# Kernel tuning notes

Measured on AMD Instinct MI355X. Metric: run time of the kernel, lower is better.

The kernel has to match this reference:

```python
import jax, jax.numpy as jnp
import numpy as np

N = 50000      # cells (nodes)
E = 800000     # kNN edges
IN = 50        # PCA dims
HID = 64       # hidden_dim
HEADS = 4
C = HID // HEADS  # per-head channels = 16
L = 3          # num_layers
NC = 12        # num_classes
INV_SQRT_C = 1.0 / np.sqrt(C)
LN_EPS = 1e-5


def setup_inputs() -> dict:
    key = jax.random.key(0)
    ks = iter(jax.random.split(key, 32))
    def w(shape, fan_in):
        return jax.random.normal(next(ks), shape, jnp.float32) / np.sqrt(fan_in)
    inp = {
        'x': jax.random.normal(next(ks), (N, IN), jnp.float32),
        'edge_index': jax.random.randint(next(ks), (2, E), 0, N, jnp.int32),
        'edge_attr': jax.random.uniform(next(ks), (E,), jnp.float32),
        # input projection
        'Win': w((IN, HID), IN), 'b_in': jnp.zeros((HID,), jnp.float32),
        # per-layer TransformerConv params (stacked over L)
        'Wq': w((L, HID, HID), HID), 'bq': jnp.zeros((L, HID), jnp.float32),
        'Wk': w((L, HID, HID), HID), 'bk': jnp.zeros((L, HID), jnp.float32),
        'Wv': w((L, HID, HID), HID), 'bv': jnp.zeros((L, HID), jnp.float32),
        'Wedge': w((L, 1, HID), 1),                      # lin_edge, bias=False
        'Wskip': w((L, HID, HID), HID), 'bskip': jnp.zeros((L, HID), jnp.float32),
        'Wbeta': w((L, 3 * HID, 1), 3 * HID),            # lin_beta, bias=False
        'ln_g': jnp.ones((L, HID), jnp.float32), 'ln_b': jnp.zeros((L, HID), jnp.float32),
        # classifier MLP
        'Wc1': w((HID, HID), HID), 'bc1': jnp.zeros((HID,), jnp.float32),
        'Wc2': w((HID, NC), HID), 'bc2': jnp.zeros((NC,), jnp.float32),
    }
    return inp


def _layer_norm(z, g, b):
    mu = z.mean(-1, keepdims=True)
    var = ((z - mu) ** 2).mean(-1, keepdims=True)
    return (z - mu) / jnp.sqrt(var + LN_EPS) * g + b


def reference(x, edge_index, edge_attr, Win, b_in, Wq, bq, Wk, bk, Wv, bv,
              Wedge, Wskip, bskip, Wbeta, ln_g, ln_b, Wc1, bc1, Wc2, bc2):
    n = x.shape[0]
    src, dst = edge_index[0], edge_index[1]   # messages flow src -> dst
    ea = edge_attr[:, None]                    # (E,1)
    h = x @ Win + b_in                         # (N,HID)
    for i in range(L):
        h_res = h
        q = (h @ Wq[i] + bq[i]).reshape(n, HEADS, C)
        k = (h @ Wk[i] + bk[i]).reshape(n, HEADS, C)
        v = (h @ Wv[i] + bv[i]).reshape(n, HEADS, C)
        e = (ea @ Wedge[i]).reshape(-1, HEADS, C)        # (E,H,C)
        kj = k[src] + e                                   # edge-gathered keys + edge feat
        alpha = jnp.einsum('ehc,ehc->eh', q[dst], kj) * INV_SQRT_C  # (E,H)
        # segment softmax over destination nodes
        amax = jax.ops.segment_max(alpha, dst, num_segments=n)
        amax = jnp.where(jnp.isfinite(amax), amax, 0.0)
        ex = jnp.exp(alpha - amax[dst])
        denom = jax.ops.segment_sum(ex, dst, num_segments=n)
        p = ex / (denom[dst] + 1e-16)
        msg = (v[src] + e) * p[..., None]                 # (E,H,C)
        out = jax.ops.segment_sum(msg, dst, num_segments=n).reshape(n, HID)
        # beta-gated skip
        x_r = h @ Wskip[i] + bskip[i]
        beta = jax.nn.sigmoid(jnp.concatenate([out, x_r, out - x_r], -1) @ Wbeta[i])  # (N,1)
        out = beta * x_r + (1.0 - beta) * out
        h = _layer_norm(out + h_res, ln_g[i], ln_b[i])
    h1 = jax.nn.relu(h @ Wc1 + bc1)
    return h1 @ Wc2 + bc2
```

## Files before the change

### kernel.cpp

```cpp
#include <hip/hip_runtime.h>
#include <hip/hip_fp16.h>
#include <math.h>

#define IN_F 50
#define HID 64
#define NC 12
#define LN_EPS 1e-5f

#define BSH 8
#define BSZ 256
#define NBK_MAX 256
#define CHUNK 8192
#define PCAP 8192

#define SCQ 0.36067376022224085f

typedef _Float16 half8 __attribute__((ext_vector_type(8)));
typedef _Float16 half4_t __attribute__((ext_vector_type(4)));
typedef _Float16 half2_t __attribute__((ext_vector_type(2)));
typedef float float4v __attribute__((ext_vector_type(4)));

static __device__ __forceinline__ half2_t h2cast(unsigned int u) {
  return __builtin_bit_cast(half2_t, u);
}

#if __has_builtin(__builtin_amdgcn_fdot2)
#define FDOT2(a, b, c) __builtin_amdgcn_fdot2((a), (b), (c), false)
#else
static __device__ __forceinline__ float FDOT2(half2_t a, half2_t b, float c) {
  return (float)a[0] * (float)b[0] + (float)a[1] * (float)b[1] + c;
}
#endif


__global__ __launch_bounds__(256) void bucket_kernel(
    const int* __restrict__ src, const int* __restrict__ dst,
    const float* __restrict__ ea, int* __restrict__ cursor,
    unsigned long long* __restrict__ rec_stage,
    unsigned short* __restrict__ dloc_stage, int e)
{
  __shared__ int bcnt[256];
  __shared__ int gbase[256];
  __shared__ int bfill[256];
  int tid = threadIdx.x;
  bcnt[tid] = 0; bfill[tid] = 0;
  __syncthreads();
  int cb = blockIdx.x * CHUNK;
  int ce = min(cb + CHUNK, e);
  for (int i = cb + tid; i < ce; i += 256)
    atomicAdd(&bcnt[dst[i] >> BSH], 1);
  __syncthreads();
  if (bcnt[tid] > 0) gbase[tid] = atomicAdd(&cursor[tid], bcnt[tid]);
  __syncthreads();
  for (int i = cb + tid; i < ce; i += 256) {
    int d = dst[i];
    int b = d >> BSH;
    int slot = atomicAdd(&bfill[b], 1);
    size_t pos = (size_t)b * PCAP + gbase[b] + slot;
    rec_stage[pos] =
        ((unsigned long long)__float_as_uint(ea[i]) << 32) | (unsigned int)src[i];
    dloc_stage[pos] = (unsigned short)(d & (BSZ - 1));
  }
}

__global__ __launch_bounds__(256) void scanb_kernel(
    const int* __restrict__ cursor, int* __restrict__ bbase,
    int* __restrict__ rowptr_n, int nbk)
{
  int t = threadIdx.x;
  int v = (t < nbk) ? cursor[t] : 0;
  int incl = v;
#pragma unroll
  for (int off = 1; off < 64; off <<= 1) {
    int tv = __shfl_up(incl, off);
    if ((t & 63) >= off) incl += tv;
  }
  __shared__ int ws[4];
  if ((t & 63) == 63) ws[t >> 6] = incl;
  __syncthreads();
  int wb = 0;
  int w = t >> 6;
#pragma unroll
  for (int j = 0; j < 4; j++) if (j < w) wb += ws[j];
  int excl = incl - v + wb;
  if (t < nbk) bbase[t] = excl;
  if (t == 255) *rowptr_n = excl;
}

__global__ __launch_bounds__(256) void place_kernel(
    const int* __restrict__ cursor, const int* __restrict__ bbase,
    const unsigned long long* __restrict__ rec_stage,
    const unsigned short* __restrict__ dloc_stage,
    unsigned long long* __restrict__ edges, int* __restrict__ rowptr, int n)
{
  extern __shared__ char smem[];
  unsigned long long* sbuf = (unsigned long long*)smem;
  int* hist = (int*)(smem + (size_t)PCAP * 8);
  int* lcnt = hist + 256;
  __shared__ int ws[4];
  int b = blockIdx.x;
  int t = threadIdx.x;
  int lo = b * BSZ;
  int hi = min(lo + BSZ, n);
  int cnt  = cursor[b];
  int base = bbase[b];
  size_t bofs = (size_t)b * PCAP;
  hist[t] = 0;
  __syncthreads();
  for (int i = t; i < cnt; i += 256)
    atomicAdd(&hist[dloc_stage[bofs + i]], 1);
  __syncthreads();
  int v = hist[t];
  int incl = v;
#pragma unroll
  for (int off = 1; off < 64; off <<= 1) {
    int tv = __shfl_up(incl, off);
    if ((t & 63) >= off) incl += tv;
  }
  if ((t & 63) == 63) ws[t >> 6] = incl;
  __syncthreads();
  int wb = 0;
  int w = t >> 6;
#pragma unroll
  for (int j = 0; j < 4; j++) if (j < w) wb += ws[j];
  int excl = incl - v + wb;
  if (lo + t < hi) rowptr[lo + t] = base + excl;
  lcnt[t] = excl;
  __syncthreads();
  for (int i = t; i < cnt; i += 256) {
    unsigned long long rec = rec_stage[bofs + i];
    int dl = dloc_stage[bofs + i];
    int slot = atomicAdd(&lcnt[dl], 1);
    sbuf[slot] = rec;
  }
  __syncthreads();
  for (int i = t; i < cnt; i += 256)
    edges[(size_t)base + i] = sbuf[i];
}


__global__ __launch_bounds__(256) void wprep_kernel(
    const float* __restrict__ Wq, const float* __restrict__ Wk,
    const float* __restrict__ Wv, const float* __restrict__ Ws,
    const float* __restrict__ Wc1, const float* __restrict__ Win,
    const float* __restrict__ bq, const float* __restrict__ bk,
    const float* __restrict__ bv, const float* __restrict__ bs,
    const float* __restrict__ bc1, const float* __restrict__ bin,
    _Float16* __restrict__ Wt, float* __restrict__ biasP)
{
  int idx = blockIdx.x * 256 + threadIdx.x;
  if (idx >= 896 * 64) return;
  int col = idx >> 6, k = idx & 63;
  float w, b;
  if (col < 768) {
    int l = col >> 8, rem = col & 255;
    int mat = rem >> 6, c = rem & 63;
    const float* W  = (mat == 0) ? Wq : (mat == 1) ? Wk : (mat == 2) ? Wv : Ws;
    const float* bb = (mat == 0) ? bq : (mat == 1) ? bk : (mat == 2) ? bv : bs;
    w = W[((size_t)l * 64 + k) * 64 + c];
    b = bb[l * 64 + c];
  } else if (col < 832) {
    int c = col - 768;
    w = Wc1[k * 64 + c];
    b = bc1[c];
  } else {
    int c = col - 832;
    w = (k < IN_F) ? Win[k * 64 + c] : 0.f;
    b = bin[c];
  }
  Wt[idx] = (_Float16)w;
  if (k == 0) biasP[col] = b;
}


template<int NMAT, int MODE, bool RELU>
__global__ __launch_bounds__(256) void gemm_mfma(
    const float* __restrict__ A, int lda, int kin, int M,
    const _Float16* __restrict__ Wt, const float* __restrict__ biasP,
    float* __restrict__ C, int ldc,
    __half* __restrict__ qxh, __half* __restrict__ kvb)
{
  __shared__ __align__(16) _Float16 hsh[64 * 72];
  constexpr int KVSZ = (MODE == 1) ? 64 * 128 : 8;
  __shared__ __align__(16) __half kvsh[KVSZ];
  __shared__ __align__(16) __half qxsh[KVSZ];

  const int tid = threadIdx.x;
  const int wave = tid >> 6, lane = tid & 63;
  const int lrow = lane & 15, quad = lane >> 4;
  const int row0 = blockIdx.x * 64;
  constexpr int WPC = 4 / NMAT;
  const int cg = wave / WPC;
  const int wi = wave % WPC;

  half8 bf[4][2];
  const _Float16* wbase = Wt + (size_t)cg * 64 * 64;
#pragma unroll
  for (int ct = 0; ct < 4; ct++)
#pragma unroll
    for (int ks = 0; ks < 2; ks++)
      bf[ct][ks] = *(const half8*)&wbase[(ct * 16 + lrow) * 64 + ks * 32 + quad * 8];
  float bv_[4];
#pragma unroll
  for (int ct = 0; ct < 4; ct++) bv_[ct] = biasP[cg * 64 + ct * 16 + lrow];

  if (kin == 64) {
    int r = tid >> 2, cq = tid & 3;
    int grow = row0 + r;
#pragma unroll
    for (int i = 0; i < 4; i++) {
      int c0 = cq * 16 + i * 4;
      float4 v = make_float4(0.f, 0.f, 0.f, 0.f);
      if (grow < M) v = *(const float4*)&A[(size_t)grow * lda + c0];
      half4_t hv;
      hv[0] = (_Float16)v.x; hv[1] = (_Float16)v.y;
      hv[2] = (_Float16)v.z; hv[3] = (_Float16)v.w;
      *(half4_t*)&hsh[r * 72 + c0] = hv;
    }
  } else {
    for (int idx = tid; idx < 64 * 64; idx += 256) {
      int r = idx >> 6, c = idx & 63;
      int grow = row0 + r;
      float v = (grow < M && c < kin) ? A[(size_t)grow * lda + c] : 0.f;
      hsh[r * 72 + c] = (_Float16)v;
    }
  }
  __syncthreads();

  float4v acc[NMAT][4];
#pragma unroll
  for (int rt = 0; rt < NMAT; rt++)
#pragma unroll
    for (int ct = 0; ct < 4; ct++) {
      acc[rt][ct][0] = bv_[ct]; acc[rt][ct][1] = bv_[ct];
      acc[rt][ct][2] = bv_[ct]; acc[rt][ct][3] = bv_[ct];
    }

#pragma unroll
  for (int rt = 0; rt < NMAT; rt++) {
    int rbase = (wi * NMAT + rt) * 16;
#pragma unroll
    for (int ks = 0; ks < 2; ks++) {
      half8 af = *(const half8*)&hsh[(rbase + lrow) * 72 + ks * 32 + quad * 8];
#pragma unroll
      for (int ct = 0; ct < 4; ct++)
        acc[rt][ct] = __builtin_amdgcn_mfma_f32_16x16x32_f16(af, bf[ct][ks],
                                                             acc[rt][ct], 0, 0, 0);
    }
  }

  if (MODE == 0) {
#pragma unroll
    for (int rt = 0; rt < NMAT; rt++) {
      int rbase = (wi * NMAT + rt) * 16;
#pragma unroll
      for (int reg = 0; reg < 4; reg++) {
        int row = row0 + rbase + quad * 4 + reg;
        if (row < M) {
#pragma unroll
          for (int ct = 0; ct < 4; ct++) {
            float v = acc[rt][ct][reg];
            if (RELU) v = fmaxf(v, 0.f);
            C[(size_t)row * ldc + cg * 64 + ct * 16 + lrow] = v;
          }
        }
      }
    }
  } else {
    __half* dstsh = (cg == 0 || cg == 3) ? qxsh : kvsh;
    int cofs = (cg == 0 || cg == 1) ? 0 : 64;
    float scale = (cg == 0) ? SCQ : 1.f;
#pragma unroll
    for (int rt = 0; rt < 4; rt++)
#pragma unroll
      for (int reg = 0; reg < 4; reg++) {
        int rloc = rt * 16 + quad * 4 + reg;
#pragma unroll
        for (int ct = 0; ct < 4; ct++)
          dstsh[rloc * 128 + cofs + ct * 16 + lrow] =
              __float2half(acc[rt][ct][reg] * scale);
      }
    __syncthreads();
    for (int idx = tid; idx < 1024; idx += 256) {
      int r = idx >> 4, c4 = idx & 15;
      int grow = row0 + r;
      if (grow < M) {
        uint2 kk = *(const uint2*)&kvsh[r * 128 + c4 * 4];
        uint2 vv = *(const uint2*)&kvsh[r * 128 + 64 + c4 * 4];
        uint4 o; o.x = kk.x; o.y = kk.y; o.z = vv.x; o.w = vv.y;
        *(uint4*)&kvb[(size_t)grow * 128 + c4 * 8] = o;
      }
    }
    for (int idx = tid; idx < 1024; idx += 256) {
      int r = idx >> 4, g8 = idx & 15;
      int grow = row0 + r;
      if (grow < M)
        *(uint4*)&qxh[(size_t)grow * 128 + g8 * 8] =
            *(const uint4*)&qxsh[r * 128 + g8 * 8];
    }
  }
}


__global__ __launch_bounds__(256) void attn_post_kernel(
    const int* __restrict__ rowptr, const unsigned long long* __restrict__ edges,
    const __half* __restrict__ qxh, const uint4* __restrict__ kvb,
    const float* __restrict__ wedge, const float* __restrict__ wbeta,
    const float* __restrict__ lng, const float* __restrict__ lnb,
    float* __restrict__ h, int n)
{
  int lane = threadIdx.x & 63;
  int node = blockIdx.x * 4 + (threadIdx.x >> 6);
  if (node >= n) return;
  int grp = lane >> 4;
  int c4 = lane & 15;
  const __half* qrow = qxh + (size_t)node * 128;
  uint2 qu = ((const uint2*)qrow)[c4];
  half2_t qh01 = h2cast(qu.x), qh23 = h2cast(qu.y);
  float qf0 = (float)qh01[0], qf1 = (float)qh01[1];
  float qf2 = (float)qh23[0], qf3 = (float)qh23[1];
  float4 we4 = ((const float4*)wedge)[c4];
  float qwe = qf0 * we4.x + qf1 * we4.y + qf2 * we4.z + qf3 * we4.w;
  int s0 = rowptr[node], s1 = rowptr[node + 1];
  float l = 0.f, pa = 0.f;
  float ax = 0.f, ay = 0.f, az = 0.f, aw = 0.f;
  for (int cb = s0; cb < s1; cb += 64) {
    int cnt = min(64, s1 - cb);
    unsigned long long rec64 = (lane < cnt) ? edges[cb + lane] : 0ull;
    unsigned int my_src = (unsigned int)(rec64 & 0xffffffffu);
    unsigned int my_ea  = (unsigned int)(rec64 >> 32);
#pragma unroll 2
    for (int j = 0; j * 4 < cnt; j++) {
      int sl = j * 4 + grp;
      bool valid = sl < cnt;
      int srcn   = (int)__shfl(my_src, sl);
      float a    = __uint_as_float(__shfl(my_ea, sl));
      uint4 kv = kvb[(size_t)srcn * 16 + c4];
      float prod = a * qwe;
      prod = FDOT2(qh01, h2cast(kv.x), prod);
      prod = FDOT2(qh23, h2cast(kv.y), prod);
      prod += __shfl_xor(prod, 1);
      prod += __shfl_xor(prod, 2);
      float p = valid ? exp2f(prod) : 0.f;
      half2_t v01 = h2cast(kv.z), v23 = h2cast(kv.w);
      l  += p;
      pa = fmaf(p, a, pa);
      ax = fmaf(p, (float)v01[0], ax);
      ay = fmaf(p, (float)v01[1], ay);
      az = fmaf(p, (float)v23[0], az);
      aw = fmaf(p, (float)v23[1], aw);
    }
  }
  ax += pa * we4.x; ay += pa * we4.y; az += pa * we4.z; aw += pa * we4.w;
  ax += __shfl_xor(ax, 16); ax += __shfl_xor(ax, 32);
  ay += __shfl_xor(ay, 16); ay += __shfl_xor(ay, 32);
  az += __shfl_xor(az, 16); az += __shfl_xor(az, 32);
  aw += __shfl_xor(aw, 16); aw += __shfl_xor(aw, 32);
  l  += __shfl_xor(l, 16);  l  += __shfl_xor(l, 32);
  float inv = 1.f / (l + 1e-16f);
  float ox = ax * inv, oy = ay * inv, oz = az * inv, ow = aw * inv;
  uint2 xu = ((const uint2*)(qrow + 64))[c4];
  half2_t x01 = h2cast(xu.x), x23 = h2cast(xu.y);
  float4 xr;
  xr.x = (float)x01[0]; xr.y = (float)x01[1];
  xr.z = (float)x23[0]; xr.w = (float)x23[1];
  float4 hr = ((const float4*)h)[(size_t)node * 16 + c4];
  float4 w1 = ((const float4*)wbeta)[c4];
  float4 w2 = ((const float4*)wbeta)[16 + c4];
  float4 w3 = ((const float4*)wbeta)[32 + c4];
  float sv = ox * w1.x + oy * w1.y + oz * w1.z + ow * w1.w
           + xr.x * w2.x + xr.y * w2.y + xr.z * w2.z + xr.w * w2.w
           + (ox - xr.x) * w3.x + (oy - xr.y) * w3.y
           + (oz - xr.z) * w3.z + (ow - xr.w) * w3.w;
  sv += __shfl_xor(sv, 1); sv += __shfl_xor(sv, 2);
  sv += __shfl_xor(sv, 4); sv += __shfl_xor(sv, 8);
  float beta = 1.f / (1.f + __expf(-sv));
  float zx = beta * xr.x + (1.f - beta) * ox + hr.x;
  float zy = beta * xr.y + (1.f - beta) * oy + hr.y;
  float zz = beta * xr.z + (1.f - beta) * oz + hr.z;
  float zw = beta * xr.w + (1.f - beta) * ow + hr.w;
  float mu = zx + zy + zz + zw;
  mu += __shfl_xor(mu, 1); mu += __shfl_xor(mu, 2);
  mu += __shfl_xor(mu, 4); mu += __shfl_xor(mu, 8);
  mu *= (1.f / 64.f);
  float dx = zx - mu, dy = zy - mu, dz = zz - mu, dw = zw - mu;
  float var = dx * dx + dy * dy + dz * dz + dw * dw;
  var += __shfl_xor(var, 1); var += __shfl_xor(var, 2);
  var += __shfl_xor(var, 4); var += __shfl_xor(var, 8);
  var *= (1.f / 64.f);
  float rstd = rsqrtf(var + LN_EPS);
  float4 g4 = ((const float4*)lng)[c4];
  float4 b4 = ((const float4*)lnb)[c4];
  if (grp == 0) {
    float4 res;
    res.x = dx * rstd * g4.x + b4.x;
    res.y = dy * rstd * g4.y + b4.y;
    res.z = dz * rstd * g4.z + b4.z;
    res.w = dw * rstd * g4.w + b4.w;
    ((float4*)h)[(size_t)node * 16 + c4] = res;
  }
}


__global__ __launch_bounds__(256) void cls2_kernel(const float* __restrict__ h1,
    const float* __restrict__ Wc2, const float* __restrict__ bc2,
    float* __restrict__ out, int n) {
  __shared__ float W2[HID * NC];
  __shared__ float b2[NC];
  int tid = threadIdx.x;
  for (int i = tid; i < HID * NC; i += 256) W2[i] = Wc2[i];
  if (tid < NC) b2[tid] = bc2[tid];
  __syncthreads();
  int row = blockIdx.x * 256 + tid;
  if (row >= n) return;
  float a[NC];
#pragma unroll
  for (int mm = 0; mm < NC; mm++) a[mm] = b2[mm];
  const float4* hp = (const float4*)(h1 + (size_t)row * HID);
#pragma unroll
  for (int k4 = 0; k4 < 16; k4++) {
    float4 hv = hp[k4];
    float h_[4] = {hv.x, hv.y, hv.z, hv.w};
#pragma unroll
    for (int kk = 0; kk < 4; kk++)
#pragma unroll
      for (int mm = 0; mm < NC; mm++)
        a[mm] = fmaf(h_[kk], W2[(k4 * 4 + kk) * NC + mm], a[mm]);
  }
#pragma unroll
  for (int mm = 0; mm < NC; mm++) out[(size_t)row * NC + mm] = a[mm];
}


extern "C" void kernel_launch(void* const* d_in, const int* in_sizes, int n_in,
                              void* d_out, int out_size, void* d_ws, size_t ws_size,
                              hipStream_t stream) {
  const float* x     = (const float*)d_in[0];
  const int*   eidx  = (const int*)d_in[1];
  const float* eattr = (const float*)d_in[2];
  const float* Win   = (const float*)d_in[3];
  const float* b_in  = (const float*)d_in[4];
  const float* Wq    = (const float*)d_in[5];
  const float* bq    = (const float*)d_in[6];
  const float* Wk    = (const float*)d_in[7];
  const float* bk    = (const float*)d_in[8];
  const float* Wv    = (const float*)d_in[9];
  const float* bv    = (const float*)d_in[10];
  const float* Wedge = (const float*)d_in[11];
  const float* Wskip = (const float*)d_in[12];
  const float* bskip = (const float*)d_in[13];
  const float* Wbeta = (const float*)d_in[14];
  const float* ln_g  = (const float*)d_in[15];
  const float* ln_b  = (const float*)d_in[16];
  const float* Wc1   = (const float*)d_in[17];
  const float* bc1   = (const float*)d_in[18];
  const float* Wc2   = (const float*)d_in[19];
  const float* bc2   = (const float*)d_in[20];
  float* out = (float*)d_out;

  int n = in_sizes[0] / IN_F;
  int e = in_sizes[2];
  const int* src = eidx;
  const int* dstp = eidx + e;

  char* ws = (char*)d_ws;
  size_t off = 0;
  auto alloc = [&](size_t bytes) { void* p = ws + off; off += (bytes + 255) & ~(size_t)255; return p; };
  int nbk = (n + BSZ - 1) / BSZ;

  int*    rowptr = (int*)alloc((size_t)(n + 1) * 4);
  int*    cursor = (int*)alloc(NBK_MAX * 4);
  int*    bbase  = (int*)alloc(NBK_MAX * 4);
  unsigned long long* rec_stage = (unsigned long long*)alloc((size_t)nbk * PCAP * 8);
  unsigned short*     dloc_stage = (unsigned short*)alloc((size_t)nbk * PCAP * 2);
  unsigned long long* edges = (unsigned long long*)alloc((size_t)e * 8);
  float*  h      = (float*)alloc((size_t)n * HID * 4);
  __half* qxh    = (__half*)alloc((size_t)n * 128 * 2);
  __half* kvb    = (__half*)alloc((size_t)n * 128 * 2);
  float*  h1     = (float*)alloc((size_t)n * HID * 4);
  _Float16* Wt   = (_Float16*)alloc((size_t)896 * 64 * 2);
  float*  biasP  = (float*)alloc(896 * 4);

  int mtiles = (n + 63) / 64;

  wprep_kernel<<<(896 * 64 + 255) / 256, 256, 0, stream>>>(
      Wq, Wk, Wv, Wskip, Wc1, Win, bq, bk, bv, bskip, bc1, b_in, Wt, biasP);

  (void)hipMemsetAsync(cursor, 0, NBK_MAX * 4, stream);
  bucket_kernel<<<(e + CHUNK - 1) / CHUNK, 256, 0, stream>>>(
      src, dstp, eattr, cursor, rec_stage, dloc_stage, e);
  scanb_kernel<<<1, 256, 0, stream>>>(cursor, bbase, rowptr + n, nbk);
  size_t psmem = (size_t)PCAP * 8 + 512 * 4;
  place_kernel<<<nbk, 256, psmem, stream>>>(
      cursor, bbase, rec_stage, dloc_stage, edges, rowptr, n);

  gemm_mfma<1, 0, false><<<mtiles, 256, 0, stream>>>(
      x, IN_F, IN_F, n, Wt + (size_t)832 * 64, biasP + 832, h, HID, nullptr, nullptr);

  for (int i = 0; i < 3; i++) {
    gemm_mfma<4, 1, false><<<mtiles, 256, 0, stream>>>(
        h, HID, HID, n, Wt + (size_t)i * 256 * 64, biasP + i * 256,
        nullptr, 0, qxh, kvb);
    attn_post_kernel<<<(n + 3) / 4, 256, 0, stream>>>(
        rowptr, edges, qxh, (const uint4*)kvb, Wedge + i * HID, Wbeta + i * 3 * HID,
        ln_g + i * HID, ln_b + i * HID, h, n);
  }

  gemm_mfma<1, 0, true><<<mtiles, 256, 0, stream>>>(
      h, HID, HID, n, Wt + (size_t)768 * 64, biasP + 768, h1, HID, nullptr, nullptr);
  cls2_kernel<<<(n + 255) / 256, 256, 0, stream>>>(h1, Wc2, bc2, out, n);
}
```

Measured before the change: 340.0 us.

## Fuse classifier second layer into GEMM, fold memset into wprep, add nontemporal loads

```diff
diff --git a/kernel.cpp b/kernel.cpp
--- a/kernel.cpp
+++ b/kernel.cpp
@@ -19,6 +19,7 @@
 typedef _Float16 half4_t __attribute__((ext_vector_type(4)));
 typedef _Float16 half2_t __attribute__((ext_vector_type(2)));
 typedef float float4v __attribute__((ext_vector_type(4)));
+typedef unsigned int uint2v __attribute__((ext_vector_type(2)));
 
 static __device__ __forceinline__ half2_t h2cast(unsigned int u) {
   return __builtin_bit_cast(half2_t, u);
@@ -139,17 +140,22 @@
 }
 
 
+#define NWCOL 908
+
 __global__ __launch_bounds__(256) void wprep_kernel(
     const float* __restrict__ Wq, const float* __restrict__ Wk,
     const float* __restrict__ Wv, const float* __restrict__ Ws,
     const float* __restrict__ Wc1, const float* __restrict__ Win,
+    const float* __restrict__ Wc2,
     const float* __restrict__ bq, const float* __restrict__ bk,
     const float* __restrict__ bv, const float* __restrict__ bs,
     const float* __restrict__ bc1, const float* __restrict__ bin,
-    _Float16* __restrict__ Wt, float* __restrict__ biasP)
+    const float* __restrict__ bc2,
+    _Float16* __restrict__ Wt, float* __restrict__ biasP, int* __restrict__ cursor)
 {
+  if (blockIdx.x == 0 && threadIdx.x < NBK_MAX) cursor[threadIdx.x] = 0;
   int idx = blockIdx.x * 256 + threadIdx.x;
-  if (idx >= 896 * 64) return;
+  if (idx >= NWCOL * 64) return;
   int col = idx >> 6, k = idx & 63;
   float w, b;
   if (col < 768) {
@@ -163,10 +169,14 @@
     int c = col - 768;
     w = Wc1[k * 64 + c];
     b = bc1[c];
-  } else {
+  } else if (col < 896) {
     int c = col - 832;
     w = (k < IN_F) ? Win[k * 64 + c] : 0.f;
     b = bin[c];
+  } else {
+    int c = col - 896;
+    w = Wc2[k * NC + c];
+    b = bc2[c];
   }
   Wt[idx] = (_Float16)w;
   if (k == 0) biasP[col] = b;
@@ -178,12 +188,15 @@
     const float* __restrict__ A, int lda, int kin, int M,
     const _Float16* __restrict__ Wt, const float* __restrict__ biasP,
     float* __restrict__ C, int ldc,
-    __half* __restrict__ qxh, __half* __restrict__ kvb)
+    __half* __restrict__ qxh, __half* __restrict__ kvb,
+    const _Float16* __restrict__ W2t, const float* __restrict__ b2)
 {
   __shared__ __align__(16) _Float16 hsh[64 * 72];
   constexpr int KVSZ = (MODE == 1) ? 64 * 128 : 8;
   __shared__ __align__(16) __half kvsh[KVSZ];
   __shared__ __align__(16) __half qxsh[KVSZ];
+  __shared__ __align__(4) _Float16 w2sh[NC * 64];
+  __shared__ float b2sh[NC];
 
   const int tid = threadIdx.x;
   const int wave = tid >> 6, lane = tid & 63;
@@ -204,24 +217,31 @@
 #pragma unroll
   for (int ct = 0; ct < 4; ct++) bv_[ct] = biasP[cg * 64 + ct * 16 + lrow];
 
+  if (MODE == 2) {
+    for (int i = tid; i < NC * 64; i += 256) w2sh[i] = W2t[i];
+    if (tid < NC) b2sh[tid] = b2[tid];
+  }
+
   if (kin == 64) {
     int r = tid >> 2, cq = tid & 3;
     int grow = row0 + r;
 #pragma unroll
     for (int i = 0; i < 4; i++) {
       int c0 = cq * 16 + i * 4;
-      float4 v = make_float4(0.f, 0.f, 0.f, 0.f);
-      if (grow < M) v = *(const float4*)&A[(size_t)grow * lda + c0];
+      float4v v = {0.f, 0.f, 0.f, 0.f};
+      if (grow < M)
+        v = __builtin_nontemporal_load((const float4v*)&A[(size_t)grow * lda + c0]);
       half4_t hv;
-      hv[0] = (_Float16)v.x; hv[1] = (_Float16)v.y;
-      hv[2] = (_Float16)v.z; hv[3] = (_Float16)v.w;
+      hv[0] = (_Float16)v[0]; hv[1] = (_Float16)v[1];
+      hv[2] = (_Float16)v[2]; hv[3] = (_Float16)v[3];
       *(half4_t*)&hsh[r * 72 + c0] = hv;
     }
   } else {
     for (int idx = tid; idx < 64 * 64; idx += 256) {
       int r = idx >> 6, c = idx & 63;
       int grow = row0 + r;
-      float v = (grow < M && c < kin) ? A[(size_t)grow * lda + c] : 0.f;
+      float v = (grow < M && c < kin)
+                    ? __builtin_nontemporal_load(&A[(size_t)grow * lda + c]) : 0.f;
       hsh[r * 72 + c] = (_Float16)v;
     }
   }
@@ -266,7 +286,7 @@
         }
       }
     }
-  } else {
+  } else if (MODE == 1) {
     __half* dstsh = (cg == 0 || cg == 3) ? qxsh : kvsh;
     int cofs = (cg == 0 || cg == 1) ? 0 : 64;
     float scale = (cg == 0) ? SCQ : 1.f;
@@ -298,6 +318,29 @@
         *(uint4*)&qxh[(size_t)grow * 128 + g8 * 8] =
             *(const uint4*)&qxsh[r * 128 + g8 * 8];
     }
+  } else {
+    __syncthreads();
+    int rbase = wi * 16;
+#pragma unroll
+    for (int reg = 0; reg < 4; reg++) {
+      int row = rbase + quad * 4 + reg;
+#pragma unroll
+      for (int ct = 0; ct < 4; ct++)
+        hsh[row * 72 + ct * 16 + lrow] = (_Float16)fmaxf(acc[0][ct][reg], 0.f);
+    }
+    __syncthreads();
+    int o = tid * 3;
+#pragma unroll
+    for (int t = 0; t < 3; t++, o++) {
+      int r = o / NC, c = o - (o / NC) * NC;
+      float s = b2sh[c];
+#pragma unroll
+      for (int k2 = 0; k2 < 32; k2++)
+        s = FDOT2(*(const half2_t*)&hsh[r * 72 + k2 * 2],
+                  *(const half2_t*)&w2sh[c * 64 + k2 * 2], s);
+      int grow = row0 + r;
+      if (grow < M) C[(size_t)grow * NC + c] = s;
+    }
   }
 }
 
@@ -315,8 +358,8 @@
   int grp = lane >> 4;
   int c4 = lane & 15;
   const __half* qrow = qxh + (size_t)node * 128;
-  uint2 qu = ((const uint2*)qrow)[c4];
-  half2_t qh01 = h2cast(qu.x), qh23 = h2cast(qu.y);
+  uint2v qu = __builtin_nontemporal_load(&((const uint2v*)qrow)[c4]);
+  half2_t qh01 = h2cast(qu[0]), qh23 = h2cast(qu[1]);
   float qf0 = (float)qh01[0], qf1 = (float)qh01[1];
   float qf2 = (float)qh23[0], qf3 = (float)qh23[1];
   float4 we4 = ((const float4*)wedge)[c4];
@@ -326,10 +369,11 @@
   float ax = 0.f, ay = 0.f, az = 0.f, aw = 0.f;
   for (int cb = s0; cb < s1; cb += 64) {
     int cnt = min(64, s1 - cb);
-    unsigned long long rec64 = (lane < cnt) ? edges[cb + lane] : 0ull;
+    unsigned long long rec64 = 0ull;
+    if (lane < cnt) rec64 = __builtin_nontemporal_load(&edges[cb + lane]);
     unsigned int my_src = (unsigned int)(rec64 & 0xffffffffu);
     unsigned int my_ea  = (unsigned int)(rec64 >> 32);
-#pragma unroll 2
+#pragma unroll 4
     for (int j = 0; j * 4 < cnt; j++) {
       int sl = j * 4 + grp;
       bool valid = sl < cnt;
@@ -359,8 +403,8 @@
   l  += __shfl_xor(l, 16);  l  += __shfl_xor(l, 32);
   float inv = 1.f / (l + 1e-16f);
   float ox = ax * inv, oy = ay * inv, oz = az * inv, ow = aw * inv;
-  uint2 xu = ((const uint2*)(qrow + 64))[c4];
-  half2_t x01 = h2cast(xu.x), x23 = h2cast(xu.y);
+  uint2v xu = __builtin_nontemporal_load(&((const uint2v*)(qrow + 64))[c4]);
+  half2_t x01 = h2cast(xu[0]), x23 = h2cast(xu[1]);
   float4 xr;
   xr.x = (float)x01[0]; xr.y = (float)x01[1];
   xr.z = (float)x23[0]; xr.w = (float)x23[1];
@@ -402,36 +446,6 @@
 }
 
 
-__global__ __launch_bounds__(256) void cls2_kernel(const float* __restrict__ h1,
-    const float* __restrict__ Wc2, const float* __restrict__ bc2,
-    float* __restrict__ out, int n) {
-  __shared__ float W2[HID * NC];
-  __shared__ float b2[NC];
-  int tid = threadIdx.x;
-  for (int i = tid; i < HID * NC; i += 256) W2[i] = Wc2[i];
-  if (tid < NC) b2[tid] = bc2[tid];
-  __syncthreads();
-  int row = blockIdx.x * 256 + tid;
-  if (row >= n) return;
-  float a[NC];
-#pragma unroll
-  for (int mm = 0; mm < NC; mm++) a[mm] = b2[mm];
-  const float4* hp = (const float4*)(h1 + (size_t)row * HID);
-#pragma unroll
-  for (int k4 = 0; k4 < 16; k4++) {
-    float4 hv = hp[k4];
-    float h_[4] = {hv.x, hv.y, hv.z, hv.w};
-#pragma unroll
-    for (int kk = 0; kk < 4; kk++)
-#pragma unroll
-      for (int mm = 0; mm < NC; mm++)
-        a[mm] = fmaf(h_[kk], W2[(k4 * 4 + kk) * NC + mm], a[mm]);
-  }
-#pragma unroll
-  for (int mm = 0; mm < NC; mm++) out[(size_t)row * NC + mm] = a[mm];
-}
-
-
 extern "C" void kernel_launch(void* const* d_in, const int* in_sizes, int n_in,
                               void* d_out, int out_size, void* d_ws, size_t ws_size,
                               hipStream_t stream) {
@@ -477,16 +491,15 @@
   float*  h      = (float*)alloc((size_t)n * HID * 4);
   __half* qxh    = (__half*)alloc((size_t)n * 128 * 2);
   __half* kvb    = (__half*)alloc((size_t)n * 128 * 2);
-  float*  h1     = (float*)alloc((size_t)n * HID * 4);
-  _Float16* Wt   = (_Float16*)alloc((size_t)896 * 64 * 2);
-  float*  biasP  = (float*)alloc(896 * 4);
+  _Float16* Wt   = (_Float16*)alloc((size_t)NWCOL * 64 * 2);
+  float*  biasP  = (float*)alloc(NWCOL * 4);
 
   int mtiles = (n + 63) / 64;
 
-  wprep_kernel<<<(896 * 64 + 255) / 256, 256, 0, stream>>>(
-      Wq, Wk, Wv, Wskip, Wc1, Win, bq, bk, bv, bskip, bc1, b_in, Wt, biasP);
-
-  (void)hipMemsetAsync(cursor, 0, NBK_MAX * 4, stream);
+  wprep_kernel<<<(NWCOL * 64 + 255) / 256, 256, 0, stream>>>(
+      Wq, Wk, Wv, Wskip, Wc1, Win, Wc2, bq, bk, bv, bskip, bc1, b_in, bc2,
+      Wt, biasP, cursor);
+
   bucket_kernel<<<(e + CHUNK - 1) / CHUNK, 256, 0, stream>>>(
       src, dstp, eattr, cursor, rec_stage, dloc_stage, e);
   scanb_kernel<<<1, 256, 0, stream>>>(cursor, bbase, rowptr + n, nbk);
@@ -495,18 +508,19 @@
       cursor, bbase, rec_stage, dloc_stage, edges, rowptr, n);
 
   gemm_mfma<1, 0, false><<<mtiles, 256, 0, stream>>>(
-      x, IN_F, IN_F, n, Wt + (size_t)832 * 64, biasP + 832, h, HID, nullptr, nullptr);
+      x, IN_F, IN_F, n, Wt + (size_t)832 * 64, biasP + 832, h, HID,
+      nullptr, nullptr, nullptr, nullptr);
 
   for (int i = 0; i < 3; i++) {
     gemm_mfma<4, 1, false><<<mtiles, 256, 0, stream>>>(
         h, HID, HID, n, Wt + (size_t)i * 256 * 64, biasP + i * 256,
-        nullptr, 0, qxh, kvb);
+        nullptr, 0, qxh, kvb, nullptr, nullptr);
     attn_post_kernel<<<(n + 3) / 4, 256, 0, stream>>>(
         rowptr, edges, qxh, (const uint4*)kvb, Wedge + i * HID, Wbeta + i * 3 * HID,
         ln_g + i * HID, ln_b + i * HID, h, n);
   }
 
-  gemm_mfma<1, 0, true><<<mtiles, 256, 0, stream>>>(
-      h, HID, HID, n, Wt + (size_t)768 * 64, biasP + 768, h1, HID, nullptr, nullptr);
-  cls2_kernel<<<(n + 255) / 256, 256, 0, stream>>>(h1, Wc2, bc2, out, n);
-}
+  gemm_mfma<1, 2, true><<<mtiles, 256, 0, stream>>>(
+      h, HID, HID, n, Wt + (size_t)768 * 64, biasP + 768, out, NC,
+      nullptr, nullptr, Wt + (size_t)896 * 64, biasP + 896);
+}
```

After: 356.6 us. 1.05x slower.
